# Kernel optimization log

Measured on AMD Instinct MI355X. Metric: run time of the kernel, lower is better.

Reference implementation:

```python
import jax, jax.numpy as jnp
import numpy as np

B = 512
IN_F = 512
OUT_F = 512
NOISE = 128
OUT_DIM = IN_F * OUT_F + OUT_F  # 262656
PRIOR_SCALE = 1.0


def setup_inputs() -> dict:
    key = jax.random.key(0)
    k_x, k_px, k_n, k_w, k_b, k_pw = jax.random.split(key, 6)
    x = jax.random.normal(k_x, (B, IN_F), dtype=jnp.float32)
    prior_x = jax.random.normal(k_px, (B, IN_F), dtype=jnp.float32)
    hyper_noise = jax.random.normal(k_n, (B, NOISE), dtype=jnp.float32)
    # nn.Linear default init: U(-1/sqrt(fan_in), 1/sqrt(fan_in))
    lim = 1.0 / np.sqrt(NOISE)
    hyper_W = jax.random.uniform(k_w, (OUT_DIM, NOISE), dtype=jnp.float32, minval=-lim, maxval=lim)
    hyper_b = jax.random.uniform(k_b, (OUT_DIM,), dtype=jnp.float32, minval=-lim, maxval=lim)
    # PriorHyperLinear: row-normalized gaussian weight (prior_std=1 -> identity scale), zero bias
    pw = jax.random.normal(k_pw, (OUT_DIM, NOISE), dtype=jnp.float32)
    prior_W = pw / jnp.linalg.norm(pw, axis=1, keepdims=True)
    prior_b = jnp.zeros((OUT_DIM,), dtype=jnp.float32)
    return {"x": x, "prior_x": prior_x, "hyper_noise": hyper_noise,
            "hyper_W": hyper_W, "hyper_b": hyper_b,
            "prior_W": prior_W, "prior_b": prior_b}


def _base_forward(x, params):
    # params: [B, IN_F*OUT_F + OUT_F]
    w = params[:, : IN_F * OUT_F].reshape(-1, IN_F, OUT_F)  # [B, in, out]
    b = params[:, IN_F * OUT_F:]                            # [B, out]
    # bmm([B,1,in],[B,in,out]) + bias -> squeeze -> [B, out]
    return jnp.einsum('bi,bio->bo', x, w) + b


def reference(x, prior_x, hyper_noise, hyper_W, hyper_b, prior_W, prior_b):
    params = hyper_noise @ hyper_W.T + hyper_b            # [B, OUT_DIM]
    out = _base_forward(x, params)
    prior_params = hyper_noise @ prior_W.T + prior_b      # [B, OUT_DIM]
    out = out + _base_forward(prior_x, prior_params) * PRIOR_SCALE
    return out
```

## Files before the change

### kernel.cpp

```cpp
#include <hip/hip_runtime.h>
#include <hip/hip_fp16.h>


#define MAIN_D (512*512)

typedef _Float16 half8 __attribute__((ext_vector_type(8)));
typedef float floatx4 __attribute__((ext_vector_type(4)));

static __device__ __forceinline__ unsigned pk2(float a, float b) {
    union { __half2 h; unsigned u; } c;
    c.h = __float22half2_rn(make_float2(a, b));
    return c.u;
}

__global__ __launch_bounds__(256) void reduce_kernel(
    const float* __restrict__ ws,
    const float* __restrict__ hb, const float* __restrict__ pb,
    float* __restrict__ out)
{
    const int idx = blockIdx.x * 256 + threadIdx.x;
    const int o4 = (idx * 4) & 511;
    float4 acc;
    acc.x = hb[MAIN_D + o4 + 0] + pb[MAIN_D + o4 + 0];
    acc.y = hb[MAIN_D + o4 + 1] + pb[MAIN_D + o4 + 1];
    acc.z = hb[MAIN_D + o4 + 2] + pb[MAIN_D + o4 + 2];
    acc.w = hb[MAIN_D + o4 + 3] + pb[MAIN_D + o4 + 3];
#pragma unroll
    for (int zz = 0; zz < 32; ++zz) {
        float4 v = *(const float4*)(ws + (long)zz * (512 * 512) + idx * 4);
        acc.x += v.x; acc.y += v.y; acc.z += v.z; acc.w += v.w;
    }
    *(float4*)(out + idx * 4) = acc;
}

__global__ __launch_bounds__(512, 2) void main_gemm(
    const float* __restrict__ x, const float* __restrict__ px,
    const float* __restrict__ noise,
    const float* __restrict__ hW, const float* __restrict__ hb,
    const float* __restrict__ pW, const float* __restrict__ pb,
    float* __restrict__ ws)
{
    __shared__ __attribute__((aligned(16))) _Float16 Bl[2][128 * 136];
    __shared__ __attribute__((aligned(16))) _Float16 xhl[256 * 40];

    const int t = threadIdx.x;
    const int lin  = blockIdx.x;
    const int s    = (lin >> 3) & 1;
    const int g    = ((lin >> 4) << 3) | (lin & 7);
    const int z    = g >> 2;
    const int y    = g & 3;
    const int b0   = s * 256;
    const int o0   = y * 128;
    const int branch = z >> 4;
    const int ic0  = (z & 15) * 32;
    const float* __restrict__ xsrc = branch ? px : x;
    const float* __restrict__ Ws   = branch ? pW : hW;
    const float* __restrict__ bias = branch ? pb : hb;
    const int nmacro = ((z & 15) == 0) ? 33 : 32;

#pragma unroll
    for (int k = 0; k < 4; ++k) {
        int idx = k * 512 + t;
        int bb = idx >> 3, c = (idx & 7) * 4;
        float4 v = *(const float4*)(xsrc + (b0 + bb) * 512 + ic0 + c);
        *(unsigned*)&xhl[bb * 40 + c]     = pk2(v.x, v.y);
        *(unsigned*)&xhl[bb * 40 + c + 2] = pk2(v.z, v.w);
    }
    _Float16* nzl = &Bl[0][0];
#pragma unroll
    for (int k = 0; k < 16; ++k) {
        int idx = k * 512 + t;
        int bb = idx >> 5, c = (idx & 31) * 4;
        float4 v = *(const float4*)(noise + (b0 + bb) * 128 + c);
        *(unsigned*)&nzl[bb * 136 + c]     = pk2(v.x, v.y);
        *(unsigned*)&nzl[bb * 136 + c + 2] = pk2(v.z, v.w);
    }
    __syncthreads();

    const int lane = t & 63;
    const int w    = t >> 6;
    const int wm64 = (w >> 1) * 64;
    const int wn64 = (w & 1) * 64;
    const int quad = lane >> 4;
    const int l16  = lane & 15;

    half8 nzf[4][4];
#pragma unroll
    for (int mf = 0; mf < 4; ++mf)
#pragma unroll
        for (int q = 0; q < 4; ++q)
            nzf[mf][q] = *(half8*)&nzl[(wm64 + mf * 16 + l16) * 136 + q * 32 + quad * 8];

    floatx4 acc[4][4];
#pragma unroll
    for (int a = 0; a < 4; ++a)
#pragma unroll
        for (int b = 0; b < 4; ++b) acc[a][b] = (floatx4)0.0f;

    float4 wa[4], wb[4];
    {
        const float* p = Ws + (long)(ic0 * 512 + o0) * 128;
#pragma unroll
        for (int j = 0; j < 4; ++j) {
            int c = j * 512 + t;
            int off = (c >> 4) * 128 + (c & 15) * 8;
            wa[j] = *(const float4*)(p + off);
            wb[j] = *(const float4*)(p + off + 4);
        }
    }
    __syncthreads();

    for (int m = 0; m < nmacro; ++m) {
        _Float16* buf = &Bl[m & 1][0];
#pragma unroll
        for (int j = 0; j < 4; ++j) {
            int c = j * 512 + t;
            int row = c >> 4, col8 = (c & 15) * 8;
            *(uint4*)&buf[row * 136 + col8] = make_uint4(
                pk2(wa[j].x, wa[j].y), pk2(wa[j].z, wa[j].w),
                pk2(wb[j].x, wb[j].y), pk2(wb[j].z, wb[j].w));
        }
        __syncthreads();
        if (m + 1 < nmacro) {
            long rb = (m + 1 < 32) ? (long)((ic0 + m + 1) * 512 + o0)
                                   : (long)(MAIN_D + o0);
            const float* p = Ws + rb * 128;
#pragma unroll
            for (int j = 0; j < 4; ++j) {
                int c = j * 512 + t;
                int off = (c >> 4) * 128 + (c & 15) * 8;
                wa[j] = *(const float4*)(p + off);
                wb[j] = *(const float4*)(p + off + 4);
            }
        }
        const bool isE2 = (m >= 32);
        _Float16 xs[4];
        if (!isE2) {
#pragma unroll
            for (int mf = 0; mf < 4; ++mf)
                xs[mf] = xhl[(wm64 + mf * 16 + l16) * 40 + m];
        }
#pragma unroll
        for (int q = 0; q < 4; ++q) {
            half8 bfr[4], afr[4];
#pragma unroll
            for (int nf = 0; nf < 4; ++nf)
                bfr[nf] = *(half8*)&buf[(wn64 + nf * 16 + l16) * 136 + q * 32 + quad * 8];
#pragma unroll
            for (int mf = 0; mf < 4; ++mf) {
                if (isE2) afr[mf] = nzf[mf][q];
                else {
                    half8 xv;
#pragma unroll
                    for (int j = 0; j < 8; ++j) xv[j] = xs[mf];
                    afr[mf] = nzf[mf][q] * xv;
                }
            }
#pragma unroll
            for (int mf = 0; mf < 4; ++mf)
#pragma unroll
                for (int nf = 0; nf < 4; ++nf)
                    acc[mf][nf] = __builtin_amdgcn_mfma_f32_16x16x32_f16(
                        afr[mf], bfr[nf], acc[mf][nf], 0, 0, 0);
        }
    }

    __syncthreads();
    {
        const int oo = t >> 2, kh = (t & 3) * 8;
        float tmp[8];
#pragma unroll
        for (int j = 0; j < 8; ++j)
            tmp[j] = bias[(long)(ic0 + kh + j) * 512 + o0 + oo];
        *(uint4*)&Bl[0][oo * 136 + kh] = make_uint4(
            pk2(tmp[0], tmp[1]), pk2(tmp[2], tmp[3]),
            pk2(tmp[4], tmp[5]), pk2(tmp[6], tmp[7]));
    }
    __syncthreads();
    {
        half8 afr[4], bfr[4];
#pragma unroll
        for (int mf = 0; mf < 4; ++mf)
            afr[mf] = *(half8*)&xhl[(wm64 + mf * 16 + l16) * 40 + quad * 8];
#pragma unroll
        for (int nf = 0; nf < 4; ++nf)
            bfr[nf] = *(half8*)&Bl[0][(wn64 + nf * 16 + l16) * 136 + quad * 8];
#pragma unroll
        for (int mf = 0; mf < 4; ++mf)
#pragma unroll
            for (int nf = 0; nf < 4; ++nf)
                acc[mf][nf] = __builtin_amdgcn_mfma_f32_16x16x32_f16(
                    afr[mf], bfr[nf], acc[mf][nf], 0, 0, 0);
    }

    float* wsl = ws + (long)z * (512 * 512);
#pragma unroll
    for (int mf = 0; mf < 4; ++mf)
#pragma unroll
        for (int nf = 0; nf < 4; ++nf)
#pragma unroll
            for (int r = 0; r < 4; ++r) {
                int row = b0 + wm64 + mf * 16 + quad * 4 + r;
                int col = o0 + wn64 + nf * 16 + l16;
                wsl[row * 512 + col] = acc[mf][nf][r];
            }
}

extern "C" void kernel_launch(void* const* d_in, const int* in_sizes, int n_in,
                              void* d_out, int out_size, void* d_ws, size_t ws_size,
                              hipStream_t stream) {
    const float* x  = (const float*)d_in[0];
    const float* px = (const float*)d_in[1];
    const float* nz = (const float*)d_in[2];
    const float* hW = (const float*)d_in[3];
    const float* hb = (const float*)d_in[4];
    const float* pW = (const float*)d_in[5];
    const float* pb = (const float*)d_in[6];
    float* out = (float*)d_out;
    float* ws  = (float*)d_ws;

    hipLaunchKernelGGL(main_gemm, dim3(256), dim3(512), 0, stream,
                       x, px, nz, hW, hb, pW, pb, ws);
    hipLaunchKernelGGL(reduce_kernel, dim3(256), dim3(256), 0, stream,
                       ws, hb, pb, out);
}
```

Baseline: 314.8 us.

## Prefetch weights two stages ahead and use an LDS-only barrier

Unrolls the macro loop by two with two register sets of prefetched weights, so each global weight load is issued two iterations before its LDS store. The __syncthreads is replaced by an explicit s_waitcnt lgkmcnt(0) plus s_barrier, so the barrier no longer waits on outstanding global loads. MFMA blocks are also wrapped in s_setprio. The cost is 32 extra live registers per thread under a 512x2 launch bound, which risks spills or lower occupancy.

New measurement: 359.7 us. +14.2%, slower.

```diff
diff --git a/kernel.cpp b/kernel.cpp
--- a/kernel.cpp
+++ b/kernel.cpp
@@ -32,6 +32,68 @@
     }
     *(float4*)(out + idx * 4) = acc;
 }
+
+#define MACRO_BODY(WA, WB, BUFI)                                              \
+  do {                                                                        \
+    _Float16* buf = &Bl[BUFI][0];                                             \
+    _Pragma("unroll")                                                         \
+    for (int j = 0; j < 4; ++j) {                                             \
+      int c = j * 512 + t;                                                    \
+      int row = c >> 4, col8 = (c & 15) * 8;                                  \
+      *(uint4*)&buf[row * 136 + col8] = make_uint4(                           \
+          pk2(WA[j].x, WA[j].y), pk2(WA[j].z, WA[j].w),                       \
+          pk2(WB[j].x, WB[j].y), pk2(WB[j].z, WB[j].w));                      \
+    }                                                                         \
+    if (m + 2 < nmacro) {                                                     \
+      long rb = (m + 2 < 32) ? (long)((ic0 + m + 2) * 512 + o0)               \
+                             : (long)(MAIN_D + o0);                           \
+      const float* p = Ws + rb * 128;                                         \
+      _Pragma("unroll")                                                       \
+      for (int j = 0; j < 4; ++j) {                                           \
+        int c = j * 512 + t;                                                  \
+        int off = (c >> 4) * 128 + (c & 15) * 8;                              \
+        WA[j] = *(const float4*)(p + off);                                    \
+        WB[j] = *(const float4*)(p + off + 4);                                \
+      }                                                                       \
+    }                                                                         \
+    asm volatile("" ::: "memory");                                            \
+    asm volatile("s_waitcnt lgkmcnt(0)" ::: "memory");                        \
+    __builtin_amdgcn_s_barrier();                                             \
+    __builtin_amdgcn_sched_barrier(0);                                        \
+    asm volatile("" ::: "memory");                                            \
+    const bool isE2 = (m >= 32);                                              \
+    _Float16 xs[4];                                                           \
+    if (!isE2) {                                                              \
+      _Pragma("unroll")                                                       \
+      for (int mf = 0; mf < 4; ++mf)                                          \
+        xs[mf] = xhl[(wm64 + mf * 16 + l16) * 40 + m];                        \
+    }                                                                         \
+    _Pragma("unroll")                                                         \
+    for (int q = 0; q < 4; ++q) {                                             \
+      half8 bfr[4], afr[4];                                                   \
+      _Pragma("unroll")                                                       \
+      for (int nf = 0; nf < 4; ++nf)                                          \
+        bfr[nf] = *(half8*)&buf[(wn64 + nf * 16 + l16) * 136 + q * 32 + quad * 8]; \
+      _Pragma("unroll")                                                       \
+      for (int mf = 0; mf < 4; ++mf) {                                        \
+        if (isE2) afr[mf] = nzf[mf][q];                                       \
+        else {                                                                \
+          half8 xv;                                                           \
+          _Pragma("unroll")                                                   \
+          for (int jj = 0; jj < 8; ++jj) xv[jj] = xs[mf];                     \
+          afr[mf] = nzf[mf][q] * xv;                                          \
+        }                                                                     \
+      }                                                                       \
+      __builtin_amdgcn_s_setprio(1);                                          \
+      _Pragma("unroll")                                                       \
+      for (int mf = 0; mf < 4; ++mf)                                          \
+        _Pragma("unroll")                                                     \
+        for (int nf = 0; nf < 4; ++nf)                                        \
+          acc[mf][nf] = __builtin_amdgcn_mfma_f32_16x16x32_f16(               \
+              afr[mf], bfr[nf], acc[mf][nf], 0, 0, 0);                        \
+      __builtin_amdgcn_s_setprio(0);                                          \
+    }                                                                         \
+  } while (0)
 
 __global__ __launch_bounds__(512, 2) void main_gemm(
     const float* __restrict__ x, const float* __restrict__ px,
@@ -97,72 +159,28 @@
 #pragma unroll
         for (int b = 0; b < 4; ++b) acc[a][b] = (floatx4)0.0f;
 
-    float4 wa[4], wb[4];
+    float4 wa0[4], wb0[4], wa1[4], wb1[4];
     {
-        const float* p = Ws + (long)(ic0 * 512 + o0) * 128;
+        const float* p0 = Ws + (long)(ic0 * 512 + o0) * 128;
+        const float* p1 = Ws + (long)((ic0 + 1) * 512 + o0) * 128;
 #pragma unroll
         for (int j = 0; j < 4; ++j) {
             int c = j * 512 + t;
             int off = (c >> 4) * 128 + (c & 15) * 8;
-            wa[j] = *(const float4*)(p + off);
-            wb[j] = *(const float4*)(p + off + 4);
+            wa0[j] = *(const float4*)(p0 + off);
+            wb0[j] = *(const float4*)(p0 + off + 4);
+            wa1[j] = *(const float4*)(p1 + off);
+            wb1[j] = *(const float4*)(p1 + off + 4);
         }
     }
     __syncthreads();
 
-    for (int m = 0; m < nmacro; ++m) {
-        _Float16* buf = &Bl[m & 1][0];
-#pragma unroll
-        for (int j = 0; j < 4; ++j) {
-            int c = j * 512 + t;
-            int row = c >> 4, col8 = (c & 15) * 8;
-            *(uint4*)&buf[row * 136 + col8] = make_uint4(
-                pk2(wa[j].x, wa[j].y), pk2(wa[j].z, wa[j].w),
-                pk2(wb[j].x, wb[j].y), pk2(wb[j].z, wb[j].w));
-        }
-        __syncthreads();
-        if (m + 1 < nmacro) {
-            long rb = (m + 1 < 32) ? (long)((ic0 + m + 1) * 512 + o0)
-                                   : (long)(MAIN_D + o0);
-            const float* p = Ws + rb * 128;
-#pragma unroll
-            for (int j = 0; j < 4; ++j) {
-                int c = j * 512 + t;
-                int off = (c >> 4) * 128 + (c & 15) * 8;
-                wa[j] = *(const float4*)(p + off);
-                wb[j] = *(const float4*)(p + off + 4);
-            }
-        }
-        const bool isE2 = (m >= 32);
-        _Float16 xs[4];
-        if (!isE2) {
-#pragma unroll
-            for (int mf = 0; mf < 4; ++mf)
-                xs[mf] = xhl[(wm64 + mf * 16 + l16) * 40 + m];
-        }
-#pragma unroll
-        for (int q = 0; q < 4; ++q) {
-            half8 bfr[4], afr[4];
-#pragma unroll
-            for (int nf = 0; nf < 4; ++nf)
-                bfr[nf] = *(half8*)&buf[(wn64 + nf * 16 + l16) * 136 + q * 32 + quad * 8];
-#pragma unroll
-            for (int mf = 0; mf < 4; ++mf) {
-                if (isE2) afr[mf] = nzf[mf][q];
-                else {
-                    half8 xv;
-#pragma unroll
-                    for (int j = 0; j < 8; ++j) xv[j] = xs[mf];
-                    afr[mf] = nzf[mf][q] * xv;
-                }
-            }
-#pragma unroll
-            for (int mf = 0; mf < 4; ++mf)
-#pragma unroll
-                for (int nf = 0; nf < 4; ++nf)
-                    acc[mf][nf] = __builtin_amdgcn_mfma_f32_16x16x32_f16(
-                        afr[mf], bfr[nf], acc[mf][nf], 0, 0, 0);
-        }
+    int m = 0;
+    while (true) {
+        MACRO_BODY(wa0, wb0, 0);
+        ++m; if (m >= nmacro) break;
+        MACRO_BODY(wa1, wb1, 1);
+        ++m; if (m >= nmacro) break;
     }
 
     __syncthreads();
```
